# Kernel optimization log

Measured on AMD Instinct MI355X. Metric: run time of the kernel, lower is better.

Reference implementation:

```python
import jax, jax.numpy as jnp
import numpy as np

NUM_HEADS = 16
HEAD_DIM = 64
D_MODEL = NUM_HEADS * HEAD_DIM


def setup_inputs() -> dict:
    key = jax.random.key(0)
    ks = jax.random.split(key, 7)
    B, S = 2, 2048
    q = jax.random.normal(ks[0], (B, S, D_MODEL), dtype=jnp.float32)
    k = jax.random.normal(ks[1], (B, S, D_MODEL), dtype=jnp.float32)
    v = jax.random.normal(ks[2], (B, S, D_MODEL), dtype=jnp.float32)
    scale = 1.0 / np.sqrt(D_MODEL).astype(np.float32)
    w_q = jax.random.normal(ks[3], (D_MODEL, D_MODEL), dtype=jnp.float32) * scale
    w_k = jax.random.normal(ks[4], (D_MODEL, D_MODEL), dtype=jnp.float32) * scale
    w_v = jax.random.normal(ks[5], (D_MODEL, D_MODEL), dtype=jnp.float32) * scale
    w_o = jax.random.normal(ks[6], (D_MODEL, D_MODEL), dtype=jnp.float32) * scale
    return {"q": q, "k": k, "v": v, "w_q": w_q, "w_k": w_k, "w_v": w_v, "w_o": w_o}


def reference(q, k, v, w_q, w_k, w_v, w_o):
    B, S, _ = q.shape
    H, D = NUM_HEADS, HEAD_DIM
    # projections; q scaled by 1/sqrt(dim) as in the original (dim = per-head dim)
    qh = (q @ w_q) / jnp.sqrt(jnp.asarray(D, q.dtype))
    kh = k @ w_k
    vh = v @ w_v
    # tf.split(axis=-1) into H chunks == reshape [B,S,H,D]
    qh = qh.reshape(B, S, H, D)
    kh = kh.reshape(B, S, H, D)
    vh = vh.reshape(B, S, H, D)
    # keras Attention: scores = q @ k^T, softmax over keys, @ v (no extra scale)
    scores = jnp.einsum("bqhd,bkhd->bhqk", qh, kh)
    probs = jax.nn.softmax(scores, axis=-1)
    o = jnp.einsum("bhqk,bkhd->bqhd", probs, vh)
    o = o.reshape(B, S, H * D)
    return o @ w_o
```

## Files before the change

kernel.cpp:

```cpp
#include <hip/hip_runtime.h>
#include <hip/hip_bf16.h>


using bf16x8 = __attribute__((ext_vector_type(8))) short;
using f32x4  = __attribute__((ext_vector_type(4))) float;
using u32x4  = __attribute__((ext_vector_type(4))) unsigned;
typedef unsigned short u16;
using u16x4 = __attribute__((ext_vector_type(4))) u16;
using u16x8 = __attribute__((ext_vector_type(8))) u16;

#define GLDS16(g, l) __builtin_amdgcn_global_load_lds( \
    (const __attribute__((address_space(1))) void*)(g), \
    (__attribute__((address_space(3))) void*)(l), 16, 0, 0)

#if __has_builtin(__builtin_amdgcn_exp2f)
#define EXP2(x) __builtin_amdgcn_exp2f(x)
#else
#define EXP2(x) exp2f(x)
#endif

__device__ __forceinline__ void block_sync() {
  __builtin_amdgcn_sched_barrier(0);
  asm volatile("" ::: "memory");
  __builtin_amdgcn_s_barrier();
  asm volatile("" ::: "memory");
  __builtin_amdgcn_sched_barrier(0);
}

__device__ __forceinline__ u16 f2bf(float f) {
  unsigned u = __builtin_bit_cast(unsigned, f);
  u += 0x7fffu + ((u >> 16) & 1u);
  return (u16)(u >> 16);
}

__device__ __forceinline__ unsigned cvt_pk_bf16(float lo, float hi) {
  unsigned r;
  asm("v_cvt_pk_bf16_f32 %0, %1, %2" : "=v"(r) : "v"(lo), "v"(hi));
  return r;
}

__device__ __forceinline__ float fmax3(float a, float b, float c) {
  return fmaxf(fmaxf(a, b), c);
}

__global__ __launch_bounds__(256) void wtrans_kernel(
    const float* __restrict__ wq, const float* __restrict__ wk,
    const float* __restrict__ wv, const float* __restrict__ wo,
    u16* __restrict__ dst) {
  __shared__ float t[32][33];
  const int z = blockIdx.z;
  const float* src = (z == 0) ? wq : (z == 1) ? wk : (z == 2) ? wv : wo;
  u16* d = dst + (size_t)z * 1024 * 1024;
  const int tx = threadIdx.x & 31, ty = threadIdx.x >> 5;
  const int bx = blockIdx.x * 32, by = blockIdx.y * 32;
#pragma unroll
  for (int j = 0; j < 4; j++)
    t[ty + j * 8][tx] = src[(size_t)(by + ty + j * 8) * 1024 + bx + tx];
  __syncthreads();
#pragma unroll
  for (int j = 0; j < 4; j++)
    d[(size_t)(bx + ty + j * 8) * 1024 + by + tx] = f2bf(t[tx][ty + j * 8]);
}

__global__ __launch_bounds__(256) void cvt_in_kernel(
    const float* __restrict__ q, const float* __restrict__ k,
    const float* __restrict__ v, u16* __restrict__ dst) {
  const int z = blockIdx.y;
  const float* src = (z == 0) ? q : (z == 1) ? k : v;
  u16* d = dst + (size_t)z * 4096 * 1024;
  size_t i = ((size_t)blockIdx.x * 256 + threadIdx.x) * 4;
  float4 f = *(const float4*)(src + i);
  uint2 o2 = make_uint2(cvt_pk_bf16(f.x, f.y), cvt_pk_bf16(f.z, f.w));
  *(uint2*)(d + i) = o2;
}

__device__ __forceinline__ void gemm128(const u16* __restrict__ A,
                                        const u16* __restrict__ B,
                                        int arow0, int bcol0,
                                        u16* ldsA, u16* ldsB,
                                        f32x4 acc[4][4]) {
  const int tid = threadIdx.x;
  const int lane = tid & 63, wave = tid >> 6;
  const int lr = lane & 15, lg = lane >> 4;
  const int wr = (wave >> 1) * 64, wc = (wave & 1) * 64;
  for (int kt = 0; kt < 1024; kt += 64) {
#pragma unroll
    for (int i = 0; i < 4; i++) {
      int o = (i * 256 + tid) * 8;
      int row = o >> 6, ch = (o >> 3) & 7;
      int sc = (ch ^ (row & 7)) << 3;
      GLDS16(A + (size_t)(arow0 + row) * 1024 + kt + sc, &ldsA[o]);
      GLDS16(B + (size_t)(bcol0 + row) * 1024 + kt + sc, &ldsB[o]);
    }
    __syncthreads();
#pragma unroll
    for (int kk = 0; kk < 2; kk++) {
      bf16x8 af[4], bfr[4];
      const int ke = kk * 32 + lg * 8;
#pragma unroll
      for (int m = 0; m < 4; m++) {
        int row = wr + m * 16 + lr;
        af[m] = *(const bf16x8*)&ldsA[row * 64 + (ke ^ ((row & 7) << 3))];
      }
#pragma unroll
      for (int n = 0; n < 4; n++) {
        int row = wc + n * 16 + lr;
        bfr[n] = *(const bf16x8*)&ldsB[row * 64 + (ke ^ ((row & 7) << 3))];
      }
#pragma unroll
      for (int m = 0; m < 4; m++)
#pragma unroll
        for (int n = 0; n < 4; n++)
          acc[m][n] = __builtin_amdgcn_mfma_f32_16x16x32_bf16(af[m], bfr[n],
                                                              acc[m][n], 0, 0, 0);
    }
    __syncthreads();
  }
}

__global__ __launch_bounds__(256) void proj_kernel(
    const u16* __restrict__ Xb, const u16* __restrict__ WT,
    u16* __restrict__ Qh, u16* __restrict__ Kh, u16* __restrict__ Vt) {
  __shared__ u16 lds[16384];
  const int z = blockIdx.z;
  const u16* A = Xb + (size_t)z * 4096 * 1024;
  const u16* B = WT + (size_t)z * 1024 * 1024;
  const int arow0 = blockIdx.y * 128, bcol0 = blockIdx.x * 128;
  f32x4 acc[4][4] = {};
  gemm128(A, B, arow0, bcol0, lds, lds + 8192, acc);

  const int lane = threadIdx.x & 63, wave = threadIdx.x >> 6;
  const int lr = lane & 15, lg = lane >> 4;
  const int wr = (wave >> 1) * 64, wc = (wave & 1) * 64;

  if (z == 2) {
    u16* T = lds;
#pragma unroll
    for (int m = 0; m < 4; m++)
#pragma unroll
      for (int n = 0; n < 4; n++)
#pragma unroll
        for (int r = 0; r < 4; r++) {
          int sl = wr + m * 16 + lg * 4 + r;
          int cl = wc + n * 16 + lr;
          T[cl * 128 + (sl ^ ((cl & 7) << 3))] = f2bf(acc[m][n][r]);
        }
    __syncthreads();
    const int t = threadIdx.x;
    const int cl = t >> 1, s0 = (t & 1) * 64;
    const int gc = bcol0 + cl;
    const size_t vrow = ((size_t)(arow0 >> 11) * 16 + (gc >> 6)) * 64 + (gc & 63);
#pragma unroll
    for (int j = 0; j < 8; j++) {
      int sl = s0 + j * 8;
      u16x8 vv = *(const u16x8*)&T[cl * 128 + (sl ^ ((cl & 7) << 3))];
      *(u16x8*)&Vt[vrow * 2048 + (size_t)((arow0 & 2047) + sl)] = vv;
    }
  } else {
    const float scale = (z == 0) ? 0.18033688f : 1.0f;
    u16* dst = (z == 0) ? Qh : Kh;
#pragma unroll
    for (int m = 0; m < 4; m++)
#pragma unroll
      for (int n = 0; n < 4; n++)
#pragma unroll
        for (int r = 0; r < 4; r++) {
          int gr = arow0 + wr + m * 16 + lg * 4 + r;
          int gc = bcol0 + wc + n * 16 + lr;
          size_t idx = (((size_t)(gr >> 11) * 16 + (gc >> 6)) * 2048 +
                        (gr & 2047)) * 64 + (gc & 63);
          dst[idx] = f2bf(acc[m][n][r] * scale);
        }
  }
}

__global__ __launch_bounds__(512, 4) void attn_kernel(
    const u16* __restrict__ Qh, const u16* __restrict__ Kh,
    const u16* __restrict__ Vt, u16* __restrict__ Ob) {
  __shared__ u16 kt[4][64 * 64];
  __shared__ u16 vt[4][64 * 64];
  const int tid = threadIdx.x;
  const int lane = tid & 63, wave = tid >> 6;
  const int lr = lane & 15, lg = lane >> 4;
  const int id = blockIdx.x;
  const int swz = (id & 7) * 64 + (id >> 3);
  const int bh = swz >> 4;
  const int q0 = (swz & 15) * 128;
  const u16* Qb = Qh + ((size_t)bh * 2048 + q0) * 64;
  const u16* Kb = Kh + (size_t)bh * 2048 * 64;
  const u16* Vb = Vt + (size_t)bh * 64 * 2048;

  bf16x8 aq[2];
#pragma unroll
  for (int kk = 0; kk < 2; kk++)
    aq[kk] = *(const bf16x8*)(Qb + (wave * 16 + lr) * 64 + kk * 32 + lg * 8);

  const int hsw = (lr & 3) | (((lr >> 2) & 1) << 2);
  int koff[2][4];
#pragma unroll
  for (int n = 0; n < 4; n++) {
    int kr = 32 * (n >> 1) + 8 * (lr >> 2) + 4 * (n & 1) + (lr & 3);
#pragma unroll
    for (int kk = 0; kk < 2; kk++)
      koff[kk][n] = kr * 64 + ((kk * 32 + lg * 8) ^ (hsw << 3));
  }
  int voff[2][4];
#pragma unroll
  for (int n = 0; n < 4; n++) {
    int d = n * 16 + lr;
#pragma unroll
    for (int ks = 0; ks < 2; ks++)
      voff[ks][n] = d * 64 + ((ks * 32 + lg * 8) ^ ((d & 7) << 3));
  }

  const int o0 = tid * 8;
  const int srow = tid >> 3, sch = tid & 7;
  const int hk = (srow & 3) | (((srow >> 3) & 1) << 2);
  const u16* kg = Kb + (size_t)srow * 64 + ((sch ^ hk) << 3);
  const u16* vg = Vb + (size_t)srow * 2048 + ((sch ^ (srow & 7)) << 3);

  f32x4 oacc[4] = {};
  float mrun = -1e30f, lrun = 0.f;

  auto STAGE = [&](int t, int b) {
    GLDS16(kg + (size_t)t * 4096, &kt[0][0] + b * 4096 + o0);
    GLDS16(vg + t * 64, &vt[0][0] + b * 4096 + o0);
  };

  auto COMPUTE = [&](int cur) {
    f32x4 sacc[4] = {};
    __builtin_amdgcn_s_setprio(1);
#pragma unroll
    for (int kk = 0; kk < 2; kk++) {
#pragma unroll
      for (int n = 0; n < 4; n++) {
        bf16x8 ka = *(const bf16x8*)&kt[cur][koff[kk][n]];
        sacc[n] = __builtin_amdgcn_mfma_f32_16x16x32_bf16(ka, aq[kk],
                                                          sacc[n], 0, 0, 0);
      }
    }
    __builtin_amdgcn_s_setprio(0);
    float t0 = fmax3(sacc[0][0], sacc[0][1], sacc[0][2]);
    float t1 = fmax3(sacc[0][3], sacc[1][0], sacc[1][1]);
    float t2 = fmax3(sacc[1][2], sacc[1][3], sacc[2][0]);
    float t3 = fmax3(sacc[2][1], sacc[2][2], sacc[2][3]);
    float t4 = fmax3(sacc[3][0], sacc[3][1], sacc[3][2]);
    float mx = fmaxf(fmax3(t0, t1, t2), fmax3(t3, t4, sacc[3][3]));
    mx = fmaxf(mx, __shfl_xor(mx, 16));
    mx = fmaxf(mx, __shfl_xor(mx, 32));
    float mnew = fmaxf(mrun, mx);
    if (__all(mx - mrun <= 8.0f)) {
      mnew = mrun;
    } else {
      float corr = EXP2(mrun - mnew);
      mrun = mnew;
      lrun *= corr;
      float cr[4];
#pragma unroll
      for (int r = 0; r < 4; r++) cr[r] = __shfl(corr, lg * 4 + r);
#pragma unroll
      for (int n = 0; n < 4; n++)
#pragma unroll
        for (int r = 0; r < 4; r++) oacc[n][r] *= cr[r];
    }
    float psum = 0.f;
#pragma unroll
    for (int n = 0; n < 4; n++)
#pragma unroll
      for (int r = 0; r < 4; r++) {
        float p = EXP2(sacc[n][r] - mnew);
        sacc[n][r] = p;
        psum += p;
      }
    psum += __shfl_xor(psum, 16);
    psum += __shfl_xor(psum, 32);
    lrun += psum;
    u32x4 w0 = {cvt_pk_bf16(sacc[0][0], sacc[0][1]),
                cvt_pk_bf16(sacc[0][2], sacc[0][3]),
                cvt_pk_bf16(sacc[1][0], sacc[1][1]),
                cvt_pk_bf16(sacc[1][2], sacc[1][3])};
    u32x4 w1 = {cvt_pk_bf16(sacc[2][0], sacc[2][1]),
                cvt_pk_bf16(sacc[2][2], sacc[2][3]),
                cvt_pk_bf16(sacc[3][0], sacc[3][1]),
                cvt_pk_bf16(sacc[3][2], sacc[3][3])};
    bf16x8 pa0 = __builtin_bit_cast(bf16x8, w0);
    bf16x8 pa1 = __builtin_bit_cast(bf16x8, w1);
    __builtin_amdgcn_s_setprio(1);
#pragma unroll
    for (int ks = 0; ks < 2; ks++) {
      bf16x8 ap = ks ? pa1 : pa0;
      bf16x8 bv[4];
#pragma unroll
      for (int n = 0; n < 4; n++)
        bv[n] = *(const bf16x8*)&vt[cur][voff[ks][n]];
#pragma unroll
      for (int n = 0; n < 4; n++)
        oacc[n] = __builtin_amdgcn_mfma_f32_16x16x32_bf16(ap, bv[n],
                                                          oacc[n], 0, 0, 0);
    }
    __builtin_amdgcn_s_setprio(0);
  };

#define VMC6 asm volatile("s_waitcnt vmcnt(6)" ::: "memory")
#define VMC4 asm volatile("s_waitcnt vmcnt(4)" ::: "memory")
#define VMC2 asm volatile("s_waitcnt vmcnt(2)" ::: "memory")
#define VMC0 asm volatile("s_waitcnt vmcnt(0)" ::: "memory")
  STAGE(0, 0); STAGE(1, 1); STAGE(2, 2);
  for (int t = 0; t < 28; t += 4) {
    STAGE(t + 3, 3); VMC6; block_sync(); COMPUTE(0); block_sync();
    STAGE(t + 4, 0); VMC6; block_sync(); COMPUTE(1); block_sync();
    STAGE(t + 5, 1); VMC6; block_sync(); COMPUTE(2); block_sync();
    STAGE(t + 6, 2); VMC6; block_sync(); COMPUTE(3); block_sync();
  }
  STAGE(31, 3); VMC6; block_sync(); COMPUTE(0); block_sync();
  VMC4; block_sync(); COMPUTE(1); block_sync();
  VMC2; block_sync(); COMPUTE(2); block_sync();
  VMC0; block_sync(); COMPUTE(3);
#undef VMC6
#undef VMC4
#undef VMC2
#undef VMC0

  const int b = bh >> 4, h = bh & 15;
  float inv = 1.0f / lrun;
  float ivr[4];
#pragma unroll
  for (int r = 0; r < 4; r++) ivr[r] = __shfl(inv, lg * 4 + r);
#pragma unroll
  for (int r = 0; r < 4; r++) {
    int qrow = q0 + wave * 16 + lg * 4 + r;
#pragma unroll
    for (int n = 0; n < 4; n++) {
      int d = n * 16 + lr;
      Ob[((size_t)b * 2048 + qrow) * 1024 + h * 64 + d] = f2bf(oacc[n][r] * ivr[r]);
    }
  }
}

__global__ __launch_bounds__(256) void outproj_kernel(
    const u16* __restrict__ Ob, const u16* __restrict__ WoT,
    float* __restrict__ out) {
  __shared__ u16 ldsA[128 * 64];
  __shared__ u16 ldsB[64 * 64];
  const int tid = threadIdx.x;
  const int lane = tid & 63, wave = tid >> 6;
  const int lr = lane & 15, lg = lane >> 4;
  const int wr = (wave >> 1) * 64;
  const int wc = (wave & 1) * 32;
  const int arow0 = blockIdx.y * 128, bcol0 = blockIdx.x * 64;
  f32x4 acc[4][2] = {};
  for (int kt = 0; kt < 1024; kt += 64) {
#pragma unroll
    for (int i = 0; i < 4; i++) {
      int o = (i * 256 + tid) * 8;
      int row = o >> 6, ch = (o >> 3) & 7;
      int sc = (ch ^ (row & 7)) << 3;
      GLDS16(Ob + (size_t)(arow0 + row) * 1024 + kt + sc, &ldsA[o]);
    }
#pragma unroll
    for (int i = 0; i < 2; i++) {
      int o = (i * 256 + tid) * 8;
      int row = o >> 6, ch = (o >> 3) & 7;
      int sc = (ch ^ (row & 7)) << 3;
      GLDS16(WoT + (size_t)(bcol0 + row) * 1024 + kt + sc, &ldsB[o]);
    }
    __syncthreads();
#pragma unroll
    for (int kk = 0; kk < 2; kk++) {
      const int ke = kk * 32 + lg * 8;
      bf16x8 af[4], bfr[2];
#pragma unroll
      for (int m = 0; m < 4; m++) {
        int row = wr + m * 16 + lr;
        af[m] = *(const bf16x8*)&ldsA[row * 64 + (ke ^ ((row & 7) << 3))];
      }
#pragma unroll
      for (int n = 0; n < 2; n++) {
        int row = wc + n * 16 + lr;
        bfr[n] = *(const bf16x8*)&ldsB[row * 64 + (ke ^ ((row & 7) << 3))];
      }
#pragma unroll
      for (int m = 0; m < 4; m++)
#pragma unroll
        for (int n = 0; n < 2; n++)
          acc[m][n] = __builtin_amdgcn_mfma_f32_16x16x32_bf16(af[m], bfr[n],
                                                              acc[m][n], 0, 0, 0);
    }
    __syncthreads();
  }
#pragma unroll
  for (int m = 0; m < 4; m++)
#pragma unroll
    for (int n = 0; n < 2; n++)
#pragma unroll
      for (int r = 0; r < 4; r++) {
        int gr = arow0 + wr + m * 16 + lg * 4 + r;
        int gc = bcol0 + wc + n * 16 + lr;
        out[(size_t)gr * 1024 + gc] = acc[m][n][r];
      }
}

extern "C" void kernel_launch(void* const* d_in, const int* in_sizes, int n_in,
                              void* d_out, int out_size, void* d_ws, size_t ws_size,
                              hipStream_t stream) {
  const float* q  = (const float*)d_in[0];
  const float* k  = (const float*)d_in[1];
  const float* v  = (const float*)d_in[2];
  const float* wq = (const float*)d_in[3];
  const float* wk = (const float*)d_in[4];
  const float* wv = (const float*)d_in[5];
  const float* wo = (const float*)d_in[6];
  float* out = (float*)d_out;
  char* ws = (char*)d_ws;

  u16* WT = (u16*)ws;
  u16* Xb = (u16*)(ws + (size_t)8  * 1024 * 1024);
  u16* Qh = (u16*)(ws + (size_t)32 * 1024 * 1024);
  u16* Kh = (u16*)(ws + (size_t)40 * 1024 * 1024);
  u16* Vt = (u16*)(ws + (size_t)48 * 1024 * 1024);
  u16* Ob = (u16*)(ws + (size_t)56 * 1024 * 1024);

  wtrans_kernel<<<dim3(32, 32, 4), 256, 0, stream>>>(wq, wk, wv, wo, WT);
  cvt_in_kernel<<<dim3(4096, 3), 256, 0, stream>>>(q, k, v, Xb);
  proj_kernel<<<dim3(8, 32, 3), 256, 0, stream>>>(Xb, WT, Qh, Kh, Vt);
  attn_kernel<<<dim3(512), 512, 0, stream>>>(Qh, Kh, Vt, Ob);
  outproj_kernel<<<dim3(16, 32), 256, 0, stream>>>(Ob, WT + (size_t)3 * 1024 * 1024, out);
}
```

Baseline: 132.7 us.

## Fuse fp32-to-bf16 input conversion into projection GEMM and remap blocks per XCD

Removes the separate cvt_in kernel. The projection GEMM now loads fp32 q/k/v directly, converts each tile to bf16 in registers and stores it swizzled into LDS. This saves a full write and re-read of the bf16 activation copy plus one launch, at the cost of synchronous register loads instead of async global-to-LDS loads for the A tile. Both the projection and output-projection grids are flattened to 1D with an XCD-aware mapping, so that blocks sharing rows of A land on the same XCD for better L2 reuse.

Result: faster. 128.5 us (-3.1%).

```diff
diff --git a/kernel.cpp b/kernel.cpp
--- a/kernel.cpp
+++ b/kernel.cpp
@@ -62,35 +62,46 @@
     d[(size_t)(bx + ty + j * 8) * 1024 + by + tx] = f2bf(t[tx][ty + j * 8]);
 }
 
-__global__ __launch_bounds__(256) void cvt_in_kernel(
-    const float* __restrict__ q, const float* __restrict__ k,
-    const float* __restrict__ v, u16* __restrict__ dst) {
-  const int z = blockIdx.y;
-  const float* src = (z == 0) ? q : (z == 1) ? k : v;
-  u16* d = dst + (size_t)z * 4096 * 1024;
-  size_t i = ((size_t)blockIdx.x * 256 + threadIdx.x) * 4;
-  float4 f = *(const float4*)(src + i);
-  uint2 o2 = make_uint2(cvt_pk_bf16(f.x, f.y), cvt_pk_bf16(f.z, f.w));
-  *(uint2*)(d + i) = o2;
-}
-
-__device__ __forceinline__ void gemm128(const u16* __restrict__ A,
-                                        const u16* __restrict__ B,
-                                        int arow0, int bcol0,
-                                        u16* ldsA, u16* ldsB,
-                                        f32x4 acc[4][4]) {
+__global__ __launch_bounds__(256) void proj_kernel(
+    const float* __restrict__ qf, const float* __restrict__ kf,
+    const float* __restrict__ vf, const u16* __restrict__ WT,
+    u16* __restrict__ Qh, u16* __restrict__ Kh, u16* __restrict__ Vt) {
+  __shared__ u16 lds[16384];
+  u16* ldsA = lds;
+  u16* ldsB = lds + 8192;
+  const int id = blockIdx.x;
+  const int xcd = id & 7, l = id >> 3;
+  const int z = l >> 5, rem = l & 31;
+  const int by = xcd * 4 + (rem >> 3);
+  const int bx = rem & 7;
+  const int arow0 = by * 128, bcol0 = bx * 128;
+  const float* A = (z == 0) ? qf : (z == 1) ? kf : vf;
+  const u16* Bw = WT + (size_t)z * 1024 * 1024;
+
   const int tid = threadIdx.x;
   const int lane = tid & 63, wave = tid >> 6;
   const int lr = lane & 15, lg = lane >> 4;
   const int wr = (wave >> 1) * 64, wc = (wave & 1) * 64;
+  f32x4 acc[4][4] = {};
+
   for (int kt = 0; kt < 1024; kt += 64) {
 #pragma unroll
     for (int i = 0; i < 4; i++) {
       int o = (i * 256 + tid) * 8;
       int row = o >> 6, ch = (o >> 3) & 7;
       int sc = (ch ^ (row & 7)) << 3;
-      GLDS16(A + (size_t)(arow0 + row) * 1024 + kt + sc, &ldsA[o]);
-      GLDS16(B + (size_t)(bcol0 + row) * 1024 + kt + sc, &ldsB[o]);
+      GLDS16(Bw + (size_t)(bcol0 + row) * 1024 + kt + sc, &ldsB[o]);
+    }
+#pragma unroll
+    for (int i = 0; i < 4; i++) {
+      int o = (i * 256 + tid) * 8;
+      int row = o >> 6, ch = (o >> 3) & 7;
+      const float* ap = A + (size_t)(arow0 + row) * 1024 + kt + ch * 8;
+      float4 f0 = *(const float4*)ap;
+      float4 f1 = *(const float4*)(ap + 4);
+      u32x4 w = {cvt_pk_bf16(f0.x, f0.y), cvt_pk_bf16(f0.z, f0.w),
+                 cvt_pk_bf16(f1.x, f1.y), cvt_pk_bf16(f1.z, f1.w)};
+      *(u32x4*)&ldsA[row * 64 + ((ch ^ (row & 7)) << 3)] = w;
     }
     __syncthreads();
 #pragma unroll
@@ -116,22 +127,6 @@
     }
     __syncthreads();
   }
-}
-
-__global__ __launch_bounds__(256) void proj_kernel(
-    const u16* __restrict__ Xb, const u16* __restrict__ WT,
-    u16* __restrict__ Qh, u16* __restrict__ Kh, u16* __restrict__ Vt) {
-  __shared__ u16 lds[16384];
-  const int z = blockIdx.z;
-  const u16* A = Xb + (size_t)z * 4096 * 1024;
-  const u16* B = WT + (size_t)z * 1024 * 1024;
-  const int arow0 = blockIdx.y * 128, bcol0 = blockIdx.x * 128;
-  f32x4 acc[4][4] = {};
-  gemm128(A, B, arow0, bcol0, lds, lds + 8192, acc);
-
-  const int lane = threadIdx.x & 63, wave = threadIdx.x >> 6;
-  const int lr = lane & 15, lg = lane >> 4;
-  const int wr = (wave >> 1) * 64, wc = (wave & 1) * 64;
 
   if (z == 2) {
     u16* T = lds;
@@ -347,7 +342,11 @@
   const int lr = lane & 15, lg = lane >> 4;
   const int wr = (wave >> 1) * 64;
   const int wc = (wave & 1) * 32;
-  const int arow0 = blockIdx.y * 128, bcol0 = blockIdx.x * 64;
+  const int id = blockIdx.x;
+  const int xcd = id & 7, l = id >> 3;
+  const int by = xcd * 4 + (l >> 4);
+  const int bx = l & 15;
+  const int arow0 = by * 128, bcol0 = bx * 64;
   f32x4 acc[4][2] = {};
   for (int kt = 0; kt < 1024; kt += 64) {
 #pragma unroll
@@ -414,15 +413,13 @@
   char* ws = (char*)d_ws;
 
   u16* WT = (u16*)ws;
-  u16* Xb = (u16*)(ws + (size_t)8  * 1024 * 1024);
   u16* Qh = (u16*)(ws + (size_t)32 * 1024 * 1024);
   u16* Kh = (u16*)(ws + (size_t)40 * 1024 * 1024);
   u16* Vt = (u16*)(ws + (size_t)48 * 1024 * 1024);
   u16* Ob = (u16*)(ws + (size_t)56 * 1024 * 1024);
 
   wtrans_kernel<<<dim3(32, 32, 4), 256, 0, stream>>>(wq, wk, wv, wo, WT);
-  cvt_in_kernel<<<dim3(4096, 3), 256, 0, stream>>>(q, k, v, Xb);
-  proj_kernel<<<dim3(8, 32, 3), 256, 0, stream>>>(Xb, WT, Qh, Kh, Vt);
+  proj_kernel<<<dim3(768), 256, 0, stream>>>(q, k, v, WT, Qh, Kh, Vt);
   attn_kernel<<<dim3(512), 512, 0, stream>>>(Qh, Kh, Vt, Ob);
-  outproj_kernel<<<dim3(16, 32), 256, 0, stream>>>(Ob, WT + (size_t)3 * 1024 * 1024, out);
-}
+  outproj_kernel<<<dim3(512), 256, 0, stream>>>(Ob, WT + (size_t)3 * 1024 * 1024, out);
+}
```
